# Performance work log

Hardware: AMD Instinct MI355X
Metric: run time of the kernel (lower is better)

Reference implementation:

```python
import jax, jax.numpy as jnp
import numpy as np

NX, NU, N, BATCH = 64, 32, 32, 192
NEWTON_ITERS = 2  # fixed outer Newton iterations (original loops to kkt_tol)


def setup_inputs() -> dict:
    key = jax.random.key(0)
    ks = jax.random.split(key, 8)
    x0 = jax.random.normal(ks[0], (BATCH, NX), jnp.float32)
    x = 0.1 * jax.random.normal(ks[1], (N + 1, BATCH, NX), jnp.float32)
    u = 0.1 * jax.random.normal(ks[2], (N, BATCH, NU), jnp.float32)
    lmd = jnp.zeros((N + 1, BATCH, NX), jnp.float32)
    # linear dynamics x+ = A x + Bm u (stable-ish A)
    A = 0.9 * jnp.eye(NX, dtype=jnp.float32) + (0.1 / np.sqrt(NX)) * jax.random.normal(ks[3], (NX, NX), jnp.float32)
    Bm = jax.random.normal(ks[4], (NX, NU), jnp.float32) / np.sqrt(NX)
    # quadratic cost weights (symmetric PD)
    Cx = jax.random.normal(ks[5], (NX, NX), jnp.float32) / np.sqrt(NX)
    Qx = Cx @ Cx.T + 0.1 * jnp.eye(NX, dtype=jnp.float32)
    Cu = jax.random.normal(ks[6], (NU, NU), jnp.float32) / np.sqrt(NU)
    Ru = Cu @ Cu.T + jnp.eye(NU, dtype=jnp.float32)
    Cf = jax.random.normal(ks[7], (NX, NX), jnp.float32) / np.sqrt(NX)
    Qf = Cf @ Cf.T + 0.1 * jnp.eye(NX, dtype=jnp.float32)
    return {"x0": x0, "x": x, "u": u, "lmd": lmd, "A": A, "Bm": Bm, "Qx": Qx, "Ru": Ru, "Qf": Qf}


def _eval_kkt(x0, x, u, lmd, A, Bm, Qx, Ru, Qf):
    # KKT residuals of the LQ OCP (GaussNewton; vectorized over stages s and batch b)
    x0res = x[0] - x0                                                   # [B,nx]
    xs = x[:-1]                                                         # [N,B,nx]
    xres = jnp.einsum('ij,sbj->sbi', A, xs) + jnp.einsum('ij,sbj->sbi', Bm, u) - x[1:]
    lx = jnp.einsum('ij,sbj->sbi', Qx, xs) + jnp.einsum('ji,sbj->sbi', A, lmd[1:]) - lmd[:-1]
    lu = jnp.einsum('ij,sbj->sbi', Ru, u) + jnp.einsum('ji,sbj->sbi', Bm, lmd[1:])
    lxN = jnp.einsum('ij,bj->bi', Qf, x[-1]) - lmd[-1]                  # terminal gradient residual
    return x0res, xres, lx, lu, lxN


def _riccati(x0res, xres, lx, lu, lxN, A, Bm, Qx, Ru, Qf):
    B_, nx = x0res.shape
    PN = jnp.broadcast_to(Qf, (B_, nx, nx))

    def bwd(carry, inp):
        P, p = carry
        lx_i, lu_i, xres_i = inp
        PA = jnp.einsum('bij,jk->bik', P, A)
        PB = jnp.einsum('bij,jk->bik', P, Bm)
        Qxx = Qx[None] + jnp.einsum('ji,bjk->bik', A, PA)
        Quu = Ru[None] + jnp.einsum('ji,bjk->bik', Bm, PB)
        Qxu = jnp.einsum('ji,bjk->bik', A, PB)
        w = jnp.einsum('bij,bj->bi', P, xres_i) + p
        qx = lx_i + jnp.einsum('ji,bj->bi', A, w)
        qu = lu_i + jnp.einsum('ji,bj->bi', Bm, w)
        rhs = jnp.concatenate([jnp.swapaxes(Qxu, 1, 2), qu[..., None]], axis=2)
        sol = -jnp.linalg.solve(Quu, rhs)
        K, k = sol[..., :nx], sol[..., nx]
        Pn = Qxx + jnp.einsum('bxi,biy->bxy', Qxu, K)
        Pn = 0.5 * (Pn + jnp.swapaxes(Pn, 1, 2))
        pn = qx + jnp.einsum('bxi,bi->bx', Qxu, k)
        return (Pn, pn), (Pn, pn, K, k)

    (_, _), (Ps, ps, Ks, ks) = jax.lax.scan(bwd, (PN, lxN), (lx, lu, xres), reverse=True)
    Ps = jnp.concatenate([Ps, PN[None]], axis=0)   # [N+1,B,nx,nx]
    ps = jnp.concatenate([ps, lxN[None]], axis=0)  # [N+1,B,nx]

    def fwd(dx, inp):
        K, k, xres_i = inp
        du = jnp.einsum('bux,bx->bu', K, dx) + k
        dxn = jnp.einsum('ij,bj->bi', A, dx) + jnp.einsum('ij,bj->bi', Bm, du) + xres_i
        return dxn, (dx, du)

    dxN, (dxs, dus) = jax.lax.scan(fwd, -x0res, (Ks, ks, xres))
    dxs = jnp.concatenate([dxs, dxN[None]], axis=0)
    dlmd = jnp.einsum('sbij,sbj->sbi', Ps, dxs) + ps
    return dxs, dus, dlmd


def _solve(x0, x, u, lmd, A, Bm, Qx, Ru, Qf):
    for _ in range(NEWTON_ITERS):
        x0res, xres, lx, lu, lxN = _eval_kkt(x0, x, u, lmd, A, Bm, Qx, Ru, Qf)
        dx, du, dlmd = _riccati(x0res, xres, lx, lu, lxN, A, Bm, Qx, Ru, Qf)
        x = x + dx
        u = u + du
        lmd = lmd + dlmd
    return x, u, lmd


def reference(x0, x, u, lmd, A, Bm, Qx, Ru, Qf):
    # returns the optimized control trajectory u* [N,B,nu]
    return _solve(x0, x, u, lmd, A, Bm, Qx, Ru, Qf)[1]
```

## Files before the change

kernel.cpp:

```cpp
#include <hip/hip_runtime.h>

#define DEV __device__ __forceinline__

constexpr int NX = 64, NU = 32, NH = 32, NB = 192;

constexpr int WS_P  = 0;
constexpr int WS_QI = WS_P  + (NH + 1) * NX * NX;
constexpr int WS_X  = WS_QI + NH * NU * NU;
constexpr int WS_K  = WS_X  + NH * NX * NU;

typedef __attribute__((ext_vector_type(8))) short bf16x8;
typedef __attribute__((ext_vector_type(4))) float f32x4;
typedef __attribute__((ext_vector_type(4))) unsigned short us4;

constexpr int LVL_M2T = 96 * 72 * 2;
constexpr int LVL_P   = 64 * 72 * 2;
constexpr int LVL_TT  = 64 * 72 * 2;
constexpr int LVL_XU  = 64 * 40 * 2;
constexpr int LVL_KT  = 64 * 40 * 2;
constexpr int LVL_QI  = 32 * 40 * 2;
constexpr int oM2T = 0;
constexpr int oP   = oM2T + 3 * LVL_M2T;
constexpr int oTT  = oP   + 3 * LVL_P;
constexpr int oXU  = oTT  + 3 * LVL_TT;
constexpr int oKT  = oXU  + 3 * LVL_XU;
constexpr int oQI  = oKT  + 3 * LVL_KT;
constexpr int oQXX = oQI  + 3 * LVL_QI;
constexpr int SMEMB = oQXX + 64 * 68 * 4;

DEV unsigned short bfh(float x) {
  unsigned u = __float_as_uint(x);
  return (unsigned short)((u + 0x7FFFu + ((u >> 16) & 1u)) >> 16);
}
DEV float bf2f(unsigned short h) { return __uint_as_float(((unsigned)h) << 16); }
DEV void split3(float x, unsigned short& h, unsigned short& m, unsigned short& l) {
  h = bfh(x); float r1 = x - bf2f(h);
  m = bfh(r1); float r2 = r1 - bf2f(m);
  l = bfh(r2);
}
DEV float4 ld4(const float* p) { return *reinterpret_cast<const float4*>(p); }
DEV void   st4(float* p, float4 v) { *reinterpret_cast<float4*>(p) = v; }
DEV void st4_nt(float* p, f32x4 v) {
  __builtin_nontemporal_store(v, (f32x4*)p);
}
DEV float  dot4(float4 a, float4 b) {
  return fmaf(a.x, b.x, fmaf(a.y, b.y, fmaf(a.z, b.z, a.w * b.w)));
}
DEV void fma4(float4& a, float s, float4 b) {
  a.x = fmaf(s, b.x, a.x); a.y = fmaf(s, b.y, a.y);
  a.z = fmaf(s, b.z, a.z); a.w = fmaf(s, b.w, a.w);
}
DEV void fma8(float* acc, float s, float4 b0, float4 b1) {
  acc[0] = fmaf(s, b0.x, acc[0]); acc[1] = fmaf(s, b0.y, acc[1]);
  acc[2] = fmaf(s, b0.z, acc[2]); acc[3] = fmaf(s, b0.w, acc[3]);
  acc[4] = fmaf(s, b1.x, acc[4]); acc[5] = fmaf(s, b1.y, acc[5]);
  acc[6] = fmaf(s, b1.z, acc[6]); acc[7] = fmaf(s, b1.w, acc[7]);
}

#define MFMA16(a, b, c) __builtin_amdgcn_mfma_f32_16x16x32_bf16(a, b, c, 0, 0, 0)

DEV f32x4 prod33(const char* A, int ao, int LA, const char* B, int bo, int LB,
                 f32x4 acc) {
  const bf16x8 a0 = *(const bf16x8*)(A + ao);
  const bf16x8 a1 = *(const bf16x8*)(A + LA + ao);
  const bf16x8 a2 = *(const bf16x8*)(A + 2 * LA + ao);
  const bf16x8 b0 = *(const bf16x8*)(B + bo);
  const bf16x8 b1 = *(const bf16x8*)(B + LB + bo);
  const bf16x8 b2 = *(const bf16x8*)(B + 2 * LB + bo);
  acc = MFMA16(a1, b1, acc);
  acc = MFMA16(a2, b0, acc);
  acc = MFMA16(a0, b2, acc);
  acc = MFMA16(a1, b0, acc);
  acc = MFMA16(a0, b1, acc);
  acc = MFMA16(a0, b0, acc);
  return acc;
}
DEV void st_pack3(char* base, int lvl, int el, f32x4 v) {
  us4 h, m, l;
#pragma unroll
  for (int r = 0; r < 4; ++r) {
    unsigned short hh, mm, ll; split3(v[r], hh, mm, ll);
    h[r] = (short)hh; m[r] = (short)mm; l[r] = (short)ll;
  }
  *(us4*)(base + el * 2) = h;
  *(us4*)(base + lvl + el * 2) = m;
  *(us4*)(base + 2 * lvl + el * 2) = l;
}

DEV void producer(char* smem, const float* Ag, const float* Bg,
                  const float* Qxg, const float* Rug, const float* Qfg,
                  float* ws) {
  const int t = threadIdx.x, lane = t & 63, wv = t >> 6;
  const int l15 = lane & 15, l4 = lane >> 4;

  char* M2T = smem + oM2T;
  char* Pp  = smem + oP;
  char* TT  = smem + oTT;
  char* XU  = smem + oXU;
  char* KT  = smem + oKT;
  char* QI  = smem + oQI;
  float* QXX = (float*)(smem + oQXX);
  float* QUU = (float*)(smem + oQXX);

  float* gP  = ws + WS_P;
  float* gQI = ws + WS_QI;
  float* gX  = ws + WS_X;
  float* gK  = ws + WS_K;
  int* flags = (int*)(ws + WS_P);

  for (int idx = t; idx < 96 * 64; idx += 512) {
    const int j = idx >> 6, m = idx & 63;
    const float v = (j < 64) ? Ag[m * 64 + j] : Bg[m * 32 + (j - 64)];
    unsigned short h, mi, lo; split3(v, h, mi, lo);
    const int eo = (j * 72 + m) * 2;
    *(unsigned short*)(M2T + eo) = h;
    *(unsigned short*)(M2T + LVL_M2T + eo) = mi;
    *(unsigned short*)(M2T + 2 * LVL_M2T + eo) = lo;
  }
  for (int idx = t; idx < 64 * 64; idx += 512) {
    const int r = idx >> 6, c = idx & 63;
    const float v = Qfg[idx];
    unsigned short h, mi, lo; split3(v, h, mi, lo);
    const int eo = (r * 72 + c) * 2;
    *(unsigned short*)(Pp + eo) = h;
    *(unsigned short*)(Pp + LVL_P + eo) = mi;
    *(unsigned short*)(Pp + 2 * LVL_P + eo) = lo;
    __builtin_nontemporal_store(v, gP + 32 * 4096 + idx);
  }
  __syncthreads();

  for (int s = NH - 1; s >= 0; --s) {
    {
      const int mT = wv >> 1, vT = wv & 1;
      f32x4 acc = {0.f, 0.f, 0.f, 0.f};
#pragma unroll
      for (int kp = 0; kp < 2; ++kp) {
        const int ao = ((mT * 16 + l15) * 72 + kp * 32 + l4 * 8) * 2;
        const int bo = (((4 + vT) * 16 + l15) * 72 + kp * 32 + l4 * 8) * 2;
        acc = prod33(Pp, ao, LVL_P, M2T, bo, LVL_M2T, acc);
      }
      st_pack3(TT, LVL_TT, (vT * 16 + l15) * 72 + mT * 16 + l4 * 4, acc);
    }
    __syncthreads();

    if (wv < 4) {
      const int uA = wv >> 1, uB = wv & 1;
      f32x4 acc = {0.f, 0.f, 0.f, 0.f};
#pragma unroll
      for (int kp = 0; kp < 2; ++kp) {
        const int ao = ((uA * 16 + l15) * 72 + kp * 32 + l4 * 8) * 2;
        const int bo = ((64 + uB * 16 + l15) * 72 + kp * 32 + l4 * 8) * 2;
        acc = prod33(TT, ao, LVL_TT, M2T, bo, LVL_M2T, acc);
      }
      const int c = uB * 16 + l15, u0 = uA * 16 + l4 * 4;
      const float4 rv = ld4(Rug + c * 32 + u0);
      QUU[c * 36 + u0 + 0] = acc[0] + rv.x;
      QUU[c * 36 + u0 + 1] = acc[1] + rv.y;
      QUU[c * 36 + u0 + 2] = acc[2] + rv.z;
      QUU[c * 36 + u0 + 3] = acc[3] + rv.w;
    } else {
      for (int q = wv - 4; q < 8; q += 4) {
        const int uT = q & 1, xT = q >> 1;
        f32x4 acc = {0.f, 0.f, 0.f, 0.f};
#pragma unroll
        for (int kp = 0; kp < 2; ++kp) {
          const int ao = ((uT * 16 + l15) * 72 + kp * 32 + l4 * 8) * 2;
          const int bo = ((xT * 16 + l15) * 72 + kp * 32 + l4 * 8) * 2;
          acc = prod33(TT, ao, LVL_TT, M2T, bo, LVL_M2T, acc);
        }
        const int x = xT * 16 + l15, u0 = uT * 16 + l4 * 4;
        st_pack3(XU, LVL_XU, x * 40 + u0, acc);
        st4_nt(gX + s * 2048 + x * 32 + u0, acc);
      }
    }
    __syncthreads();

    if (wv == 0) {
      const int i = lane & 31, h = lane >> 5;
      float W[16];
#pragma unroll
      for (int r = 0; r < 16; ++r) W[r] = QUU[i * 36 + h * 16 + r];
#pragma unroll
      for (int j = 0; j < 32; ++j) {
        const int jh = j >> 4, jr = j & 15;
        const float d = __shfl(W[jr], j | (jh << 5));
        const float pinv = 1.0f / d;
        const float f = __shfl(W[jr], i | (jh << 5));
        float pr[16];
#pragma unroll
        for (int r = 0; r < 16; ++r) pr[r] = __shfl(W[r], j | (h << 5));
        float nw[16];
        if (i == j) {
#pragma unroll
          for (int r = 0; r < 16; ++r) nw[r] = pr[r] * pinv;
          if (h == jh) nw[jr] = pinv;
        } else {
          const float g = f * pinv;
#pragma unroll
          for (int r = 0; r < 16; ++r) nw[r] = fmaf(-g, pr[r], W[r]);
          if (h == jh) nw[jr] = -g;
        }
#pragma unroll
        for (int r = 0; r < 16; ++r) W[r] = nw[r];
      }
#pragma unroll
      for (int q = 0; q < 4; ++q) {
        f32x4 o = {W[4 * q], W[4 * q + 1], W[4 * q + 2], W[4 * q + 3]};
        st4_nt(gQI + s * 1024 + i * 32 + h * 16 + 4 * q, o);
        st_pack3(QI, LVL_QI, i * 40 + h * 16 + 4 * q, o);
      }
    } else {
      for (int tt = wv - 1; tt < 16; tt += 7) {
        const int mT = tt & 3, jT = tt >> 2;
        f32x4 acc = {0.f, 0.f, 0.f, 0.f};
#pragma unroll
        for (int kp = 0; kp < 2; ++kp) {
          const int ao = ((mT * 16 + l15) * 72 + kp * 32 + l4 * 8) * 2;
          const int bo = ((jT * 16 + l15) * 72 + kp * 32 + l4 * 8) * 2;
          acc = prod33(Pp, ao, LVL_P, M2T, bo, LVL_M2T, acc);
        }
        st_pack3(TT, LVL_TT, (jT * 16 + l15) * 72 + mT * 16 + l4 * 4, acc);
      }
    }
    __syncthreads();

    if (t == 0) {
      __threadfence();
      __hip_atomic_store(flags + s, 1, __ATOMIC_RELEASE, __HIP_MEMORY_SCOPE_AGENT);
    }

    if (wv < 2) {
      for (int tt = wv; tt < 8; tt += 2) {
        const int mT = tt & 1, xT = tt >> 1;
        f32x4 acc = {0.f, 0.f, 0.f, 0.f};
        const int ao = ((mT * 16 + l15) * 40 + l4 * 8) * 2;
        const int bo = ((xT * 16 + l15) * 40 + l4 * 8) * 2;
        acc = prod33(QI, ao, LVL_QI, XU, bo, LVL_XU, acc);
        const int x = xT * 16 + l15, m0 = mT * 16 + l4 * 4;
#pragma unroll
        for (int r = 0; r < 4; ++r)
          __builtin_nontemporal_store(-acc[r], gK + s * 2048 + (m0 + r) * 64 + x);
        st_pack3(KT, LVL_KT, x * 40 + m0, acc);
      }
    } else {
      for (int tt = wv - 2; tt < 16; tt += 6) {
        const int jT = tt >> 2, iT = tt & 3;
        f32x4 acc = {0.f, 0.f, 0.f, 0.f};
#pragma unroll
        for (int kp = 0; kp < 2; ++kp) {
          const int ao = ((jT * 16 + l15) * 72 + kp * 32 + l4 * 8) * 2;
          const int bo = ((iT * 16 + l15) * 72 + kp * 32 + l4 * 8) * 2;
          acc = prod33(TT, ao, LVL_TT, M2T, bo, LVL_M2T, acc);
        }
        const int c = iT * 16 + l15, j0 = jT * 16 + l4 * 4;
        const float4 q = ld4(Qxg + c * 64 + j0);
        QXX[c * 68 + j0 + 0] = acc[0] + q.x;
        QXX[c * 68 + j0 + 1] = acc[1] + q.y;
        QXX[c * 68 + j0 + 2] = acc[2] + q.z;
        QXX[c * 68 + j0 + 3] = acc[3] + q.w;
      }
    }
    __syncthreads();

    if (s > 0) {
      for (int tt = wv; tt < 16; tt += 8) {
        const int iT = tt & 3, jT = tt >> 2;
        f32x4 acc = {0.f, 0.f, 0.f, 0.f};
        const int ao = ((iT * 16 + l15) * 40 + l4 * 8) * 2;
        const int bo = ((jT * 16 + l15) * 40 + l4 * 8) * 2;
        acc = prod33(XU, ao, LVL_XU, KT, bo, LVL_KT, acc);
        const int j = jT * 16 + l15, i0 = iT * 16 + l4 * 4;
        f32x4 pv;
#pragma unroll
        for (int r = 0; r < 4; ++r) {
          pv[r] = QXX[(i0 + r) * 68 + j] - acc[r];
          __builtin_nontemporal_store(pv[r], gP + s * 4096 + (i0 + r) * 64 + j);
        }
        st_pack3(Pp, LVL_P, j * 72 + i0, pv);
      }
    }
    __syncthreads();
  }

  if (t == 0) {
    __threadfence();
    __hip_atomic_store(flags + 32, 1, __ATOMIC_RELEASE, __HIP_MEMORY_SCOPE_AGENT);
  }
}

DEV void consumer(float* lds, int b, const float* x0g, const float* xg,
                  const float* ug, const float* lg, const float* Ag,
                  const float* Bg, const float* Qxg, const float* Rug,
                  const float* Qfg, float* ws, float* outp) {
  const int t = threadIdx.x;
  const float* gP  = ws + WS_P;
  const float* gQI = ws + WS_QI;
  const float* gX  = ws + WS_X;
  const float* gK  = ws + WS_K;
  int* flags = (int*)(ws + WS_P);

  float* sx   = lds;
  float* sl   = lds + 2112;
  float* su   = lds + 4224;
  float* sAT  = lds;
  float* xres = lds + 5248;
  float* lxs  = lds + 7296;
  float* lus  = lds + 9344;
  float* kv   = lds + 10368;
  float* swv  = lds + 11392;
  float* sqv  = lds + 11456;
  float* sduv = lds + 11488;
  float* sdxv = lds + 11520;

  for (int idx = t; idx < (NH + 1) * NX; idx += 512) {
    const int s = idx >> 6, i = idx & 63;
    sx[idx] = xg[(s * NB + b) * NX + i];
    sl[idx] = lg[(s * NB + b) * NX + i];
  }
  for (int idx = t; idx < NH * NU; idx += 512) {
    const int s = idx >> 5, j = idx & 31;
    su[idx] = ug[(s * NB + b) * NU + j];
  }
  __syncthreads();

  if (t < 256) {
    const int s = t >> 3, i0 = (t & 7) * 8;
    float accx[8], accl[8];
#pragma unroll
    for (int ii = 0; ii < 8; ++ii) {
      accx[ii] = -sx[(s + 1) * NX + i0 + ii];
      accl[ii] = -sl[s * NX + i0 + ii];
    }
#pragma unroll 2
    for (int k0 = 0; k0 < NX; k0 += 4) {
      const float4 xv = ld4(sx + s * NX + k0);
#pragma unroll
      for (int ii = 0; ii < 8; ++ii) {
        accx[ii] += dot4(ld4(Ag + (i0 + ii) * NX + k0), xv);
        accl[ii] += dot4(ld4(Qxg + (i0 + ii) * NX + k0), xv);
      }
    }
#pragma unroll 2
    for (int k0 = 0; k0 < NU; k0 += 4) {
      const float4 uv = ld4(su + s * NU + k0);
#pragma unroll
      for (int ii = 0; ii < 8; ++ii)
        accx[ii] += dot4(ld4(Bg + (i0 + ii) * NU + k0), uv);
    }
#pragma unroll 4
    for (int k = 0; k < NX; ++k) {
      const float lv = sl[(s + 1) * NX + k];
      fma8(accl, lv, ld4(Ag + k * NX + i0), ld4(Ag + k * NX + i0 + 4));
    }
#pragma unroll
    for (int ii = 0; ii < 8; ++ii) {
      xres[s * NX + i0 + ii] = accx[ii];
      lxs[s * NX + i0 + ii] = accl[ii];
    }
  }
  if (t < 256) {
    const int s = t >> 3, j0 = (t & 7) * 4;
    float4 acc = {0, 0, 0, 0};
#pragma unroll 2
    for (int k0 = 0; k0 < NU; k0 += 4) {
      const float4 uv = ld4(su + s * NU + k0);
      acc.x += dot4(ld4(Rug + (j0 + 0) * NU + k0), uv);
      acc.y += dot4(ld4(Rug + (j0 + 1) * NU + k0), uv);
      acc.z += dot4(ld4(Rug + (j0 + 2) * NU + k0), uv);
      acc.w += dot4(ld4(Rug + (j0 + 3) * NU + k0), uv);
    }
#pragma unroll 4
    for (int k = 0; k < NX; ++k) {
      const float lv = sl[(s + 1) * NX + k];
      fma4(acc, lv, ld4(Bg + k * NU + j0));
    }
    lus[s * NU + j0 + 0] = acc.x; lus[s * NU + j0 + 1] = acc.y;
    lus[s * NU + j0 + 2] = acc.z; lus[s * NU + j0 + 3] = acc.w;
  }

  float p_i = 0.0f, dx_i = 0.0f;
  if (t < 64) {
    const int i = t;
    float acc = -sl[NH * NX + i];
#pragma unroll 4
    for (int k0 = 0; k0 < NX; k0 += 4)
      acc += dot4(ld4(Qfg + i * NX + k0), ld4(sx + NH * NX + k0));
    p_i = acc;
    dx_i = x0g[b * NX + i] - sx[i];
  }
  __syncthreads();

  for (int idx = t; idx < NX * NX / 4; idx += 512) {
    const int k = idx >> 4, i4 = (idx & 15) * 4;
    const float4 a4 = ld4(Ag + k * NX + i4);
    sAT[(i4 + 0) * 68 + k] = a4.x;
    sAT[(i4 + 1) * 68 + k] = a4.y;
    sAT[(i4 + 2) * 68 + k] = a4.z;
    sAT[(i4 + 3) * 68 + k] = a4.w;
  }
  __syncthreads();

  if (t >= 64) return;

  const int i = t;
  const int j = t & 31;
  const int hh = t >> 5;

  for (int s = NH - 1; s >= 0; --s) {
    while (__hip_atomic_load(flags + s, __ATOMIC_RELAXED,
                             __HIP_MEMORY_SCOPE_AGENT) == 0)
      __builtin_amdgcn_s_sleep(4);
    (void)__hip_atomic_load(flags + s, __ATOMIC_ACQUIRE,
                            __HIP_MEMORY_SCOPE_AGENT);

    const float* Pr = gP + (s + 1) * NX * NX + i * NX;
    const float* xr = xres + s * NX;
    float w = p_i;
#pragma unroll
    for (int k0 = 0; k0 < NX; k0 += 16) {
      w += dot4(ld4(Pr + k0),      ld4(xr + k0));
      w += dot4(ld4(Pr + k0 + 4),  ld4(xr + k0 + 4));
      w += dot4(ld4(Pr + k0 + 8),  ld4(xr + k0 + 8));
      w += dot4(ld4(Pr + k0 + 12), ld4(xr + k0 + 12));
    }
    swv[i] = w;

    float qx = lxs[s * NX + i];
#pragma unroll
    for (int k0 = 0; k0 < NX; k0 += 16) {
      qx += dot4(ld4(sAT + i * 68 + k0),      ld4(swv + k0));
      qx += dot4(ld4(sAT + i * 68 + k0 + 4),  ld4(swv + k0 + 4));
      qx += dot4(ld4(sAT + i * 68 + k0 + 8),  ld4(swv + k0 + 8));
      qx += dot4(ld4(sAT + i * 68 + k0 + 12), ld4(swv + k0 + 12));
    }

    float qa = 0.0f;
    const int kb = hh * 32;
#pragma unroll 8
    for (int kk = 0; kk < 32; ++kk)
      qa = fmaf(Bg[(kb + kk) * NU + j], swv[kb + kk], qa);
    qa += __shfl_xor(qa, 32);
    const float qu = qa + lus[s * NU + j];
    if (hh == 0) sqv[j] = qu;

    const float* Qr = gQI + s * NU * NU + j * NU + hh * 16;
    float ka = dot4(ld4(Qr),      ld4(sqv + hh * 16))
             + dot4(ld4(Qr + 4),  ld4(sqv + hh * 16 + 4))
             + dot4(ld4(Qr + 8),  ld4(sqv + hh * 16 + 8))
             + dot4(ld4(Qr + 12), ld4(sqv + hh * 16 + 12));
    ka += __shfl_xor(ka, 32);
    if (hh == 0) kv[s * NU + j] = -ka;

    const float* Xs = gX + s * 2048 + i * 32;
    float pp = qx;
#pragma unroll
    for (int m0 = 0; m0 < NU; m0 += 4)
      pp += dot4(ld4(Xs + m0), ld4(kv + s * NU + m0));
    p_i = pp;
  }

  while (__hip_atomic_load(flags + 32, __ATOMIC_RELAXED,
                           __HIP_MEMORY_SCOPE_AGENT) == 0)
    __builtin_amdgcn_s_sleep(4);
  (void)__hip_atomic_load(flags + 32, __ATOMIC_ACQUIRE,
                          __HIP_MEMORY_SCOPE_AGENT);

  sdxv[i] = dx_i;
  for (int s = 0; s < NH; ++s) {
    const float* Kr = gK + s * NU * NX + j * NX + hh * 32;
    const float* dxh = sdxv + hh * 32;
    float da = 0.0f;
#pragma unroll
    for (int k0 = 0; k0 < 32; k0 += 16) {
      da += dot4(ld4(Kr + k0),      ld4(dxh + k0));
      da += dot4(ld4(Kr + k0 + 4),  ld4(dxh + k0 + 4));
      da += dot4(ld4(Kr + k0 + 8),  ld4(dxh + k0 + 8));
      da += dot4(ld4(Kr + k0 + 12), ld4(dxh + k0 + 12));
    }
    da += __shfl_xor(da, 32);
    const float du = da + kv[s * NU + j];
    if (hh == 0) {
      const int gi = (s * NB + b) * NU + j;
      outp[gi] = ug[gi] + du;
      sduv[j] = du;
    }

    float nxv = xres[s * NX + i];
    const float* Ar = Ag + i * NX;
#pragma unroll
    for (int k0 = 0; k0 < NX; k0 += 4)
      nxv += dot4(ld4(Ar + k0), ld4(sdxv + k0));
    const float* Br = Bg + i * NU;
#pragma unroll
    for (int m0 = 0; m0 < NU; m0 += 4)
      nxv += dot4(ld4(Br + m0), ld4(sduv + m0));
    sdxv[i] = nxv;
  }
}

__global__ void k_zero(float* ws) {
  if (threadIdx.x < 64) ((int*)(ws + WS_P))[threadIdx.x] = 0;
}

__global__ __launch_bounds__(512) void k_fused(
    const float* __restrict__ x0g, const float* __restrict__ xg,
    const float* __restrict__ ug, const float* __restrict__ lg,
    const float* __restrict__ Ag, const float* __restrict__ Bg,
    const float* __restrict__ Qxg, const float* __restrict__ Rug,
    const float* __restrict__ Qfg, float* __restrict__ ws,
    float* __restrict__ outp) {
  __shared__ __align__(16) char smem[SMEMB];
  if (blockIdx.x == 0)
    producer(smem, Ag, Bg, Qxg, Rug, Qfg, ws);
  else
    consumer((float*)smem, blockIdx.x - 1, x0g, xg, ug, lg, Ag, Bg, Qxg, Rug,
             Qfg, ws, outp);
}

extern "C" void kernel_launch(void* const* d_in, const int* in_sizes, int n_in,
                              void* d_out, int out_size, void* d_ws, size_t ws_size,
                              hipStream_t stream) {
  const float* x0  = (const float*)d_in[0];
  const float* x   = (const float*)d_in[1];
  const float* u   = (const float*)d_in[2];
  const float* lmd = (const float*)d_in[3];
  const float* A   = (const float*)d_in[4];
  const float* Bm  = (const float*)d_in[5];
  const float* Qx  = (const float*)d_in[6];
  const float* Ru  = (const float*)d_in[7];
  const float* Qf  = (const float*)d_in[8];
  float* ws  = (float*)d_ws;
  float* out = (float*)d_out;

  hipLaunchKernelGGL(k_zero, dim3(1), dim3(64), 0, stream, ws);
  hipLaunchKernelGGL(k_fused, dim3(NB + 1), dim3(512), 0, stream,
                     x0, x, u, lmd, A, Bm, Qx, Ru, Qf, ws, out);
}
```

Baseline: 412.7 us.

## Restructure Riccati producer stages and drop final completion flag wait

The producer now computes P*[A|B] in a single fused stage, so the separate P*A stage is gone. Qxx is staged in a global scratch buffer instead of LDS. The gain K is computed by all waves before the per-stage flag is released. The consumer no longer waits for a global all-done flag before its forward pass and relies on the per-stage flags instead, which lets the forward rollout start earlier. The risks are that the global scratch round-trip for Qxx is now on the critical path, and that removing the __threadfence weakens the memory-ordering guarantees.

```diff
diff --git a/kernel.cpp b/kernel.cpp
--- a/kernel.cpp
+++ b/kernel.cpp
@@ -4,10 +4,11 @@
 
 constexpr int NX = 64, NU = 32, NH = 32, NB = 192;
 
-constexpr int WS_P  = 0;
-constexpr int WS_QI = WS_P  + (NH + 1) * NX * NX;
-constexpr int WS_X  = WS_QI + NH * NU * NU;
-constexpr int WS_K  = WS_X  + NH * NX * NU;
+constexpr int WS_P   = 0;
+constexpr int WS_QI  = WS_P  + (NH + 1) * NX * NX;
+constexpr int WS_X   = WS_QI + NH * NU * NU;
+constexpr int WS_K   = WS_X  + NH * NX * NU;
+constexpr int WS_STG = WS_K  + NH * NU * NX;
 
 typedef __attribute__((ext_vector_type(8))) short bf16x8;
 typedef __attribute__((ext_vector_type(4))) float f32x4;
@@ -15,7 +16,7 @@
 
 constexpr int LVL_M2T = 96 * 72 * 2;
 constexpr int LVL_P   = 64 * 72 * 2;
-constexpr int LVL_TT  = 64 * 72 * 2;
+constexpr int LVL_TT  = 96 * 72 * 2;
 constexpr int LVL_XU  = 64 * 40 * 2;
 constexpr int LVL_KT  = 64 * 40 * 2;
 constexpr int LVL_QI  = 32 * 40 * 2;
@@ -25,8 +26,8 @@
 constexpr int oXU  = oTT  + 3 * LVL_TT;
 constexpr int oKT  = oXU  + 3 * LVL_XU;
 constexpr int oQI  = oKT  + 3 * LVL_KT;
-constexpr int oQXX = oQI  + 3 * LVL_QI;
-constexpr int SMEMB = oQXX + 64 * 68 * 4;
+constexpr int oQUU = oQI  + 3 * LVL_QI;
+constexpr int SMEMB = oQUU + 32 * 36 * 4;
 
 DEV unsigned short bfh(float x) {
   unsigned u = __float_as_uint(x);
@@ -99,14 +100,14 @@
   char* XU  = smem + oXU;
   char* KT  = smem + oKT;
   char* QI  = smem + oQI;
-  float* QXX = (float*)(smem + oQXX);
-  float* QUU = (float*)(smem + oQXX);
-
-  float* gP  = ws + WS_P;
-  float* gQI = ws + WS_QI;
-  float* gX  = ws + WS_X;
-  float* gK  = ws + WS_K;
-  int* flags = (int*)(ws + WS_P);
+  float* QUU = (float*)(smem + oQUU);
+
+  float* gP   = ws + WS_P;
+  float* gQI  = ws + WS_QI;
+  float* gX   = ws + WS_X;
+  float* gK   = ws + WS_K;
+  float* gStg = ws + WS_STG;
+  int* flags  = (int*)(ws + WS_P);
 
   for (int idx = t; idx < 96 * 64; idx += 512) {
     const int j = idx >> 6, m = idx & 63;
@@ -130,16 +131,21 @@
   __syncthreads();
 
   for (int s = NH - 1; s >= 0; --s) {
-    {
-      const int mT = wv >> 1, vT = wv & 1;
+#pragma unroll
+    for (int q = 0; q < 3; ++q) {
+      const int tt = wv + q * 8;
+      const int isV = tt >= 16;
+      const int t2 = isV ? tt - 16 : tt;
+      const int mT = t2 & 3;
+      const int br = (isV ? 64 : 0) + (t2 >> 2) * 16;
       f32x4 acc = {0.f, 0.f, 0.f, 0.f};
 #pragma unroll
       for (int kp = 0; kp < 2; ++kp) {
         const int ao = ((mT * 16 + l15) * 72 + kp * 32 + l4 * 8) * 2;
-        const int bo = (((4 + vT) * 16 + l15) * 72 + kp * 32 + l4 * 8) * 2;
+        const int bo = ((br + l15) * 72 + kp * 32 + l4 * 8) * 2;
         acc = prod33(Pp, ao, LVL_P, M2T, bo, LVL_M2T, acc);
       }
-      st_pack3(TT, LVL_TT, (vT * 16 + l15) * 72 + mT * 16 + l4 * 4, acc);
+      st_pack3(TT, LVL_TT, (br + l15) * 72 + mT * 16 + l4 * 4, acc);
     }
     __syncthreads();
 
@@ -148,7 +154,7 @@
       f32x4 acc = {0.f, 0.f, 0.f, 0.f};
 #pragma unroll
       for (int kp = 0; kp < 2; ++kp) {
-        const int ao = ((uA * 16 + l15) * 72 + kp * 32 + l4 * 8) * 2;
+        const int ao = ((64 + uA * 16 + l15) * 72 + kp * 32 + l4 * 8) * 2;
         const int bo = ((64 + uB * 16 + l15) * 72 + kp * 32 + l4 * 8) * 2;
         acc = prod33(TT, ao, LVL_TT, M2T, bo, LVL_M2T, acc);
       }
@@ -159,12 +165,14 @@
       QUU[c * 36 + u0 + 2] = acc[2] + rv.z;
       QUU[c * 36 + u0 + 3] = acc[3] + rv.w;
     } else {
-      for (int q = wv - 4; q < 8; q += 4) {
-        const int uT = q & 1, xT = q >> 1;
+#pragma unroll
+      for (int q = 0; q < 2; ++q) {
+        const int tt = (wv - 4) * 2 + q;
+        const int uT = tt & 1, xT = tt >> 1;
         f32x4 acc = {0.f, 0.f, 0.f, 0.f};
 #pragma unroll
         for (int kp = 0; kp < 2; ++kp) {
-          const int ao = ((uT * 16 + l15) * 72 + kp * 32 + l4 * 8) * 2;
+          const int ao = ((64 + uT * 16 + l15) * 72 + kp * 32 + l4 * 8) * 2;
           const int bo = ((xT * 16 + l15) * 72 + kp * 32 + l4 * 8) * 2;
           acc = prod33(TT, ao, LVL_TT, M2T, bo, LVL_M2T, acc);
         }
@@ -210,81 +218,66 @@
         st_pack3(QI, LVL_QI, i * 40 + h * 16 + 4 * q, o);
       }
     } else {
-      for (int tt = wv - 1; tt < 16; tt += 7) {
-        const int mT = tt & 3, jT = tt >> 2;
-        f32x4 acc = {0.f, 0.f, 0.f, 0.f};
-#pragma unroll
-        for (int kp = 0; kp < 2; ++kp) {
-          const int ao = ((mT * 16 + l15) * 72 + kp * 32 + l4 * 8) * 2;
-          const int bo = ((jT * 16 + l15) * 72 + kp * 32 + l4 * 8) * 2;
-          acc = prod33(Pp, ao, LVL_P, M2T, bo, LVL_M2T, acc);
+#pragma unroll
+      for (int q = 0; q < 3; ++q) {
+        const int tt = (wv - 1) + q * 7;
+        if (tt < 16) {
+          const int jT = tt >> 2, iT = tt & 3;
+          f32x4 acc = {0.f, 0.f, 0.f, 0.f};
+#pragma unroll
+          for (int kp = 0; kp < 2; ++kp) {
+            const int ao = ((jT * 16 + l15) * 72 + kp * 32 + l4 * 8) * 2;
+            const int bo = ((iT * 16 + l15) * 72 + kp * 32 + l4 * 8) * 2;
+            acc = prod33(TT, ao, LVL_TT, M2T, bo, LVL_M2T, acc);
+          }
+          const int c = iT * 16 + l15, j0 = jT * 16 + l4 * 4;
+          const float4 qv = ld4(Qxg + c * 64 + j0);
+          float4 o; o.x = acc[0] + qv.x; o.y = acc[1] + qv.y;
+          o.z = acc[2] + qv.z; o.w = acc[3] + qv.w;
+          st4(gStg + c * 64 + j0, o);
         }
-        st_pack3(TT, LVL_TT, (jT * 16 + l15) * 72 + mT * 16 + l4 * 4, acc);
       }
     }
     __syncthreads();
 
-    if (t == 0) {
-      __threadfence();
+    {
+      const int mT = wv & 1, xT = wv >> 1;
+      f32x4 acc = {0.f, 0.f, 0.f, 0.f};
+      const int ao = ((mT * 16 + l15) * 40 + l4 * 8) * 2;
+      const int bo = ((xT * 16 + l15) * 40 + l4 * 8) * 2;
+      acc = prod33(QI, ao, LVL_QI, XU, bo, LVL_XU, acc);
+      const int x = xT * 16 + l15, m0 = mT * 16 + l4 * 4;
+#pragma unroll
+      for (int r = 0; r < 4; ++r)
+        __builtin_nontemporal_store(-acc[r], gK + s * 2048 + (m0 + r) * 64 + x);
+      st_pack3(KT, LVL_KT, x * 40 + m0, acc);
+    }
+    __syncthreads();
+
+    if (t == 0)
       __hip_atomic_store(flags + s, 1, __ATOMIC_RELEASE, __HIP_MEMORY_SCOPE_AGENT);
-    }
-
-    if (wv < 2) {
-      for (int tt = wv; tt < 8; tt += 2) {
-        const int mT = tt & 1, xT = tt >> 1;
-        f32x4 acc = {0.f, 0.f, 0.f, 0.f};
-        const int ao = ((mT * 16 + l15) * 40 + l4 * 8) * 2;
-        const int bo = ((xT * 16 + l15) * 40 + l4 * 8) * 2;
-        acc = prod33(QI, ao, LVL_QI, XU, bo, LVL_XU, acc);
-        const int x = xT * 16 + l15, m0 = mT * 16 + l4 * 4;
-#pragma unroll
-        for (int r = 0; r < 4; ++r)
-          __builtin_nontemporal_store(-acc[r], gK + s * 2048 + (m0 + r) * 64 + x);
-        st_pack3(KT, LVL_KT, x * 40 + m0, acc);
-      }
-    } else {
-      for (int tt = wv - 2; tt < 16; tt += 6) {
-        const int jT = tt >> 2, iT = tt & 3;
-        f32x4 acc = {0.f, 0.f, 0.f, 0.f};
-#pragma unroll
-        for (int kp = 0; kp < 2; ++kp) {
-          const int ao = ((jT * 16 + l15) * 72 + kp * 32 + l4 * 8) * 2;
-          const int bo = ((iT * 16 + l15) * 72 + kp * 32 + l4 * 8) * 2;
-          acc = prod33(TT, ao, LVL_TT, M2T, bo, LVL_M2T, acc);
-        }
-        const int c = iT * 16 + l15, j0 = jT * 16 + l4 * 4;
-        const float4 q = ld4(Qxg + c * 64 + j0);
-        QXX[c * 68 + j0 + 0] = acc[0] + q.x;
-        QXX[c * 68 + j0 + 1] = acc[1] + q.y;
-        QXX[c * 68 + j0 + 2] = acc[2] + q.z;
-        QXX[c * 68 + j0 + 3] = acc[3] + q.w;
-      }
-    }
-    __syncthreads();
 
     if (s > 0) {
-      for (int tt = wv; tt < 16; tt += 8) {
+#pragma unroll
+      for (int q = 0; q < 2; ++q) {
+        const int tt = wv + q * 8;
         const int iT = tt & 3, jT = tt >> 2;
         f32x4 acc = {0.f, 0.f, 0.f, 0.f};
         const int ao = ((iT * 16 + l15) * 40 + l4 * 8) * 2;
         const int bo = ((jT * 16 + l15) * 40 + l4 * 8) * 2;
         acc = prod33(XU, ao, LVL_XU, KT, bo, LVL_KT, acc);
         const int j = jT * 16 + l15, i0 = iT * 16 + l4 * 4;
+        const float4 qx4 = ld4(gStg + j * 64 + i0);
         f32x4 pv;
-#pragma unroll
-        for (int r = 0; r < 4; ++r) {
-          pv[r] = QXX[(i0 + r) * 68 + j] - acc[r];
+        pv[0] = qx4.x - acc[0]; pv[1] = qx4.y - acc[1];
+        pv[2] = qx4.z - acc[2]; pv[3] = qx4.w - acc[3];
+#pragma unroll
+        for (int r = 0; r < 4; ++r)
           __builtin_nontemporal_store(pv[r], gP + s * 4096 + (i0 + r) * 64 + j);
-        }
         st_pack3(Pp, LVL_P, j * 72 + i0, pv);
       }
     }
     __syncthreads();
-  }
-
-  if (t == 0) {
-    __threadfence();
-    __hip_atomic_store(flags + 32, 1, __ATOMIC_RELEASE, __HIP_MEMORY_SCOPE_AGENT);
   }
 }
 
@@ -458,12 +451,6 @@
       pp += dot4(ld4(Xs + m0), ld4(kv + s * NU + m0));
     p_i = pp;
   }
-
-  while (__hip_atomic_load(flags + 32, __ATOMIC_RELAXED,
-                           __HIP_MEMORY_SCOPE_AGENT) == 0)
-    __builtin_amdgcn_s_sleep(4);
-  (void)__hip_atomic_load(flags + 32, __ATOMIC_ACQUIRE,
-                          __HIP_MEMORY_SCOPE_AGENT);
 
   sdxv[i] = dx_i;
   for (int s = 0; s < NH; ++s) {
```

Result: no change. 418.0 us (+1.3%).
